# Optimization experiments

Hardware: AMD Instinct MI355X
Metric: run time of the kernel (lower is better)

## Reference

```python
import jax, jax.numpy as jnp
import numpy as np

Nmax = 200
B = 512
LATENT = 128
ENC_H = 256
DEC_H = 512
M = 20


def setup_inputs() -> dict:
    key = jax.random.key(0)
    ks = jax.random.split(key, 16)

    def rn(k, shape):
        return jax.random.normal(k, shape, jnp.float32) / np.sqrt(shape[0]).astype(np.float32)

    inp = {}
    inp["x"] = jax.random.normal(ks[0], (Nmax + 1, B, 5), jnp.float32)
    inp["N_s"] = jax.random.randint(ks[1], (B, 1), 0, Nmax, jnp.int32)
    inp["eps"] = jax.random.normal(ks[2], (B, LATENT), jnp.float32)
    # bidirectional encoder LSTM (torch gate order i,f,g,o)
    inp["enc_Wih_f"] = rn(ks[3], (5, 4 * ENC_H))
    inp["enc_Whh_f"] = rn(ks[4], (ENC_H, 4 * ENC_H))
    inp["enc_b_f"] = jnp.zeros((4 * ENC_H,), jnp.float32)
    inp["enc_Wih_b"] = rn(ks[5], (5, 4 * ENC_H))
    inp["enc_Whh_b"] = rn(ks[6], (ENC_H, 4 * ENC_H))
    inp["enc_b_b"] = jnp.zeros((4 * ENC_H,), jnp.float32)
    inp["W_mu"] = rn(ks[7], (2 * ENC_H, LATENT))
    inp["b_mu"] = jnp.zeros((LATENT,), jnp.float32)
    inp["W_logvar"] = rn(ks[8], (2 * ENC_H, LATENT))
    inp["b_logvar"] = jnp.zeros((LATENT,), jnp.float32)
    # decoder
    inp["W_fc_in"] = rn(ks[9], (LATENT, 2 * DEC_H))
    inp["b_fc_in"] = jnp.zeros((2 * DEC_H,), jnp.float32)
    inp["dec_Wih"] = rn(ks[10], (5 + LATENT, 4 * DEC_H))
    inp["dec_Whh"] = rn(ks[11], (DEC_H, 4 * DEC_H))
    inp["dec_b"] = jnp.zeros((4 * DEC_H,), jnp.float32)
    inp["W_out"] = rn(ks[12], (DEC_H, 6 * M + 3))
    inp["b_out"] = jnp.zeros((6 * M + 3,), jnp.float32)
    return inp


def _lstm_step(h, c, x, Wih, Whh, b):
    g = x @ Wih + h @ Whh + b
    i, f, gg, o = jnp.split(g, 4, axis=-1)
    c = jax.nn.sigmoid(f) * c + jax.nn.sigmoid(i) * jnp.tanh(gg)
    h = jax.nn.sigmoid(o) * jnp.tanh(c)
    return h, c


def reference(x, N_s, eps, enc_Wih_f, enc_Whh_f, enc_b_f, enc_Wih_b, enc_Whh_b, enc_b_b,
              W_mu, b_mu, W_logvar, b_logvar, W_fc_in, b_fc_in,
              dec_Wih, dec_Whh, dec_b, W_out, b_out):
    Bn = x.shape[1]
    dt = x.dtype

    # ---- bidirectional LSTM encoder -> mean, logvar ----
    def run(xs, Wih, Whh, b):
        H = Whh.shape[0]
        def step(hc, xt):
            h, c = _lstm_step(hc[0], hc[1], xt, Wih, Whh, b)
            return (h, c), None
        (h, _), _ = jax.lax.scan(step, (jnp.zeros((Bn, H), dt), jnp.zeros((Bn, H), dt)), xs)
        return h

    h_enc = jnp.concatenate([run(x, enc_Wih_f, enc_Whh_f, enc_b_f),
                             run(x[::-1], enc_Wih_b, enc_Whh_b, enc_b_b)], axis=-1)
    mean = h_enc @ W_mu + b_mu
    logvar = h_enc @ W_logvar + b_logvar
    z = mean + jnp.exp(logvar / 2) * eps  # reparameterize

    # decoder initial state from z
    hc0 = jnp.tanh(z @ W_fc_in + b_fc_in)
    h0, c0 = jnp.split(hc0, 2, axis=-1)

    # ---- make_target ----
    lens = N_s[:, 0]  # [B]
    mask = (jnp.arange(Nmax + 1)[:, None] < lens[None, :]).astype(dt)  # [Nmax+1, B]
    dx, dy = x[..., 0], x[..., 1]

    stroke0 = jnp.broadcast_to(jnp.array([0, 0, 1, 0, 0], dt), (Bn, 5))  # SOS
    empty = jnp.array([0, 0, 0, 0, 1], dt)
    steps = jnp.arange(1, Nmax)
    xs = (x[1:Nmax], dx[1:Nmax], dy[1:Nmax], mask[1:Nmax], steps)

    def step(carry, inp):
        h, c, prev, pl, ol = carry
        xt, dxt, dyt, mt, i = inp
        h, c = _lstm_step(h, c, jnp.concatenate([prev, z], axis=-1), dec_Wih, dec_Whh, dec_b)
        y = h @ W_out + b_out  # [B, 6M+3]
        mix = y[:, :6 * M].reshape(Bn, M, 6)
        pi_h, mu_x, mu_y, sx_h, sy_h, rho_h = (mix[..., j] for j in range(6))
        q_h = y[:, 6 * M:]
        pi = jax.nn.softmax(pi_h, axis=-1)
        sx, sy, rho = jnp.exp(sx_h), jnp.exp(sy_h), jnp.tanh(rho_h)
        # pen reconstruction loss (categorical CE over p1,p2,p3)
        pl = pl + (-(xt[:, 2:] * jax.nn.log_softmax(q_h, axis=-1)).sum() / Bn) / Nmax
        # offset reconstruction loss (bivariate GMM NLL, masked)
        zx = (dxt[:, None] - mu_x) / sx
        zy = (dyt[:, None] - mu_y) / sy
        om = 1.0 - rho * rho
        pdf = jnp.exp(-(zx * zx + zy * zy - 2.0 * rho * zx * zy) / (2.0 * om)) / (2.0 * jnp.pi * sx * sy * jnp.sqrt(om))
        gmm = (pi * pdf).sum(axis=-1)
        ol = ol + (-(mt * jnp.log(gmm + 1e-6)).sum() / Bn) / Nmax
        # deterministic next stroke: expected offsets + argmax pen state
        q = jax.nn.softmax(q_h, axis=-1)
        stroke = jnp.concatenate([(pi * mu_x).sum(-1, keepdims=True),
                                  (pi * mu_y).sum(-1, keepdims=True),
                                  jax.nn.one_hot(jnp.argmax(q, axis=-1), 3, dtype=dt)], axis=-1)
        stroke = jnp.where((i > lens)[:, None], empty, stroke)  # per-index stroke masking
        return (h, c, stroke, pl, ol), stroke

    init = (h0, c0, stroke0, jnp.zeros((), dt), jnp.zeros((), dt))
    (_, _, _, pen_loss, offset_loss), strokes = jax.lax.scan(step, init, xs)
    # torch returns strokes[1:]; row Nmax is never written -> zeros
    strokes = jnp.concatenate([strokes, jnp.zeros((1, Bn, 5), dt)], axis=0)  # [Nmax, B, 5]
    return strokes, offset_loss, pen_loss, mean, logvar
```

## Files before the change

kernel.cpp:

```cpp
#include <hip/hip_runtime.h>
#include <hip/hip_bf16.h>
#include <math.h>

#define NMIX 20

typedef unsigned short u16;
typedef unsigned int   u32;
typedef unsigned long long u64;
typedef __bf16 bfx8 __attribute__((ext_vector_type(8)));
typedef float  fx4  __attribute__((ext_vector_type(4)));

#define MFMA16(a,b,c) __builtin_amdgcn_mfma_f32_16x16x32_bf16((a),(b),(c),0,0,0)

__device__ __forceinline__ float sigm(float x){ return 1.0f/(1.0f+__expf(-x)); }
__device__ __forceinline__ u16 f2bf(float x){ u32 u=__float_as_uint(x); return (u16)((u + 0x7fffu + ((u>>16)&1u))>>16); }
__device__ __forceinline__ float bf2f(u16 h){ return __uint_as_float(((u32)h)<<16); }
__device__ __forceinline__ u32 packh(float v){ u16 hh=f2bf(v); return ((u32)hh<<16) | (u32)f2bf(v - bf2f(hh)); }

__device__ __forceinline__ u64 ald64(const u64* p){ return __hip_atomic_load(p,__ATOMIC_RELAXED,__HIP_MEMORY_SCOPE_AGENT); }
__device__ __forceinline__ u32 ald32(const u32* p){ return __hip_atomic_load(p,__ATOMIC_RELAXED,__HIP_MEMORY_SCOPE_AGENT); }
__device__ __forceinline__ void ast64(u64* p,u64 v){ __hip_atomic_store(p,v,__ATOMIC_RELAXED,__HIP_MEMORY_SCOPE_AGENT); }
__device__ __forceinline__ void ast32(u32* p,u32 v){ __hip_atomic_store(p,v,__ATOMIC_RELAXED,__HIP_MEMORY_SCOPE_AGENT); }

__device__ __forceinline__ void poll(const int* f,int mask,int tok){
  const int idx=(threadIdx.x&63)&mask;
  for(;;){ int v=__hip_atomic_load(f+idx,__ATOMIC_RELAXED,__HIP_MEMORY_SCOPE_AGENT);
    if(__all(v>=tok)) break; __builtin_amdgcn_s_sleep(1); }
  __atomic_signal_fence(__ATOMIC_SEQ_CST);
}

__global__ __launch_bounds__(256) void prep_split_T(const float* __restrict__ src,
                                                    u16* dhi, u16* dlo, int K, int Nsrc, int Nout) {
    int idx = blockIdx.x * 256 + threadIdx.x;
    if (idx >= Nout * K) return;
    int n = idx / K, k = idx - n * K;
    float v = (n < Nsrc) ? src[k * Nsrc + n] : 0.0f;
    u16 hh = f2bf(v);
    dhi[idx] = hh;
    dlo[idx] = f2bf(v - bf2f(hh));
}

__global__ __launch_bounds__(256,1) void enc_persist(
    const float* __restrict__ x,
    const float* __restrict__ Wih_f, const float* __restrict__ b_f,
    const float* __restrict__ Wih_b, const float* __restrict__ b_b,
    const u16* __restrict__ encT, u32* __restrict__ he32, int* __restrict__ encF)
{
    __shared__ u16 AH[32*256];
    __shared__ u16 AL[32*256];
    __shared__ float xL[160];

    const int bx=blockIdx.x, dir=bx>>6, jx=(bx>>4)&3, rt=bx&15;
    const int j0=jx*64, row0=rt*32;
    int* ef = encF + (dir*16+rt)*32;
    const u16* wTh = encT + dir*524288;
    const u16* wTl = wTh + 262144;
    const float* Wih = dir? Wih_b : Wih_f;
    const float* bias= dir? b_b : b_f;

    const int tid=threadIdx.x, wv=tid>>6, lane=tid&63;
    const int ln15=lane&15, kq=lane>>4;
    const int jc = wv*16+ln15;
    const int arow = tid>>3, agran = tid&7;

    float wih[5][4], bi4[4];
#pragma unroll
    for(int g=0; g<4; ++g){
        bi4[g] = bias[g*256 + j0 + jc];
#pragma unroll
        for(int i=0;i<5;++i) wih[i][g] = Wih[i*1024 + g*256 + j0 + jc];
    }
    float c16[2][4] = {};

#pragma unroll 1
    for (int t=0; t<=200; ++t) {
      const int pb=t&1;
      const u32* hp = he32 + (pb*2+dir)*131072;
      u32* hn = he32 + ((pb^1)*2+dir)*131072;
      const int ts = dir ? 200-t : t;
      for (int i = tid; i < 160; i += 256) xL[i] = x[ts*2560 + row0*5 + i];
      poll(ef, 3, t);

      u64 q[16];
      {
        const u64* s = (const u64*)(hp + (size_t)(row0+arow)*256);
#pragma unroll
        for(int i=0;i<16;++i) q[i] = ald64(s + i*8 + agran);
      }
#pragma unroll
      for(int i=0;i<16;++i){
        u32 pe=(u32)q[i], po=(u32)(q[i]>>32);
        int ui = i*8 + agran;
        int off = arow*256 + (((ui>>2) ^ (arow&7))<<3) + (ui&3)*2;
        *(u32*)&AH[off] = (pe>>16) | (po & 0xffff0000u);
        *(u32*)&AL[off] = (pe & 0xffffu) | (po<<16);
      }
      __syncthreads();

      fx4 acc[2][4] = {};
#pragma unroll
      for(int ch=0; ch<8; ++ch){
        bfx8 ah[2], al[2];
#pragma unroll
        for(int rta=0;rta<2;++rta){
          int off = (rta*16+ln15)*256 + (((ch*4+kq)^(ln15&7))<<3);
          ah[rta]=*(const bfx8*)&AH[off]; al[rta]=*(const bfx8*)&AL[off];
        }
#pragma unroll
        for(int nt=0;nt<4;++nt){
          size_t bo=(size_t)(nt*256 + j0 + jc)*256 + ch*32 + kq*8;
          bfx8 bh=*(const bfx8*)&wTh[bo], bl=*(const bfx8*)&wTl[bo];
#pragma unroll
          for(int rta=0;rta<2;++rta){
            acc[rta][nt]=MFMA16(ah[rta],bh,acc[rta][nt]);
            acc[rta][nt]=MFMA16(ah[rta],bl,acc[rta][nt]);
            acc[rta][nt]=MFMA16(al[rta],bh,acc[rta][nt]);}}
      }
#pragma unroll
      for(int rta=0;rta<2;++rta)
#pragma unroll
      for(int r2=0;r2<4;++r2){
        const int rl=rta*16+kq*4+r2;
        float gv[4];
#pragma unroll
        for(int g=0;g<4;++g){
          float s2=acc[rta][g][r2]+bi4[g];
#pragma unroll
          for(int i=0;i<5;++i) s2+=xL[rl*5+i]*wih[i][g];
          gv[g]=s2;}
        float cv=c16[rta][r2];
        cv=sigm(gv[1])*cv+sigm(gv[0])*tanhf(gv[2]);
        c16[rta][r2]=cv;
        float hv2=sigm(gv[3])*tanhf(cv);
        ast32(&hn[(row0+rl)*256 + j0 + jc], packh(hv2));
      }
      __syncthreads();
      if(tid==0) __hip_atomic_store(&ef[jx], t+1, __ATOMIC_RELAXED, __HIP_MEMORY_SCOPE_AGENT);
    }
}

__global__ __launch_bounds__(256) void latent1(
    const u32* __restrict__ he32,
    const float* __restrict__ W_mu, const float* __restrict__ b_mu,
    const float* __restrict__ W_lv, const float* __restrict__ b_lv,
    const float* __restrict__ eps, float* z, float* out)
{
    __shared__ float hs[16 * 512];
    const int row0 = blockIdx.x * 16;
    const int tid = threadIdx.x;
    const u32* hf = he32 + 2*131072;
    const u32* hb = he32 + 3*131072;
    for (int i = tid; i < 8192; i += 256) {
        int r = i >> 9, col = i & 511;
        int gi = (row0 + r) * 256;
        u32 p = (col < 256) ? hf[gi + col] : hb[gi + (col - 256)];
        hs[i] = bf2f((u16)(p >> 16)) + bf2f((u16)p);
    }
    __syncthreads();
    for (int p = tid; p < 2048; p += 256) {
        int r = p >> 7, cc = p & 127;
        const float* hr = hs + r * 512;
        float m = 0, lv = 0;
#pragma unroll 8
        for (int k = 0; k < 512; ++k) {
            float hv = hr[k];
            m  += hv * W_mu[k * 128 + cc];
            lv += hv * W_lv[k * 128 + cc];
        }
        m += b_mu[cc]; lv += b_lv[cc];
        int b = row0 + r;
        out[512002 + b * 128 + cc] = m;
        out[577538 + b * 128 + cc] = lv;
        z[b * 128 + cc] = m + __expf(0.5f * lv) * eps[b * 128 + cc];
    }
}

__global__ __launch_bounds__(256) void latent2(
    const float* __restrict__ z, const float* __restrict__ W_fc, const float* __restrict__ b_fc,
    const float* __restrict__ dWih, const float* __restrict__ dec_b,
    u32* __restrict__ hd32, float* c_d, float* zpre)
{
    __shared__ float zs[16 * 128];
    const int row0 = blockIdx.y * 16;
    const int tid = threadIdx.x;
    {
        float4* dst = (float4*)zs;
        const float4* src = (const float4*)(z + row0 * 128);
        for (int i = tid; i < 512; i += 256) dst[i] = src[i];
    }
    __syncthreads();
    const int colbase = blockIdx.x * 128;
    for (int p = tid; p < 16 * 128; p += 256) {
        int r = p >> 7, cl = p & 127;
        int col = colbase + cl;
        const float* zr = zs + r * 128;
        int b = row0 + r;
        if (col < 1024) {
            float acc = 0;
#pragma unroll 8
            for (int k = 0; k < 128; ++k) acc += zr[k] * W_fc[k * 1024 + col];
            float v = tanhf(acc + b_fc[col]);
            if (col < 512) hd32[b * 512 + col] = packh(v);
            else           c_d[b * 512 + (col - 512)] = v;
        } else {
            int n = col - 1024;
            float acc = 0;
#pragma unroll 8
            for (int k = 0; k < 128; ++k) acc += zr[k] * dWih[(5 + k) * 2048 + n];
            zpre[b * 2048 + n] = acc + dec_b[n];
        }
    }
}

__global__ __launch_bounds__(256,1) void dec_persist(
    const float* __restrict__ x, const int* __restrict__ N_s,
    const float* __restrict__ dec_Wih, const float* __restrict__ b_out,
    const u16* __restrict__ decT, const u16* __restrict__ woutT,
    const float* __restrict__ zpre, const float* __restrict__ c_init,
    u32* __restrict__ hd32, float* __restrict__ sxsG, float* __restrict__ out,
    int* __restrict__ decHF, int* __restrict__ decSF)
{
    __shared__ u16 AH[32*256];
    __shared__ u16 AL[32*256];
    __shared__ float sxsL[32*8];
    __shared__ float xtL[160];
    __shared__ float yL[32*132];
    __shared__ int  lenL[32];
    __shared__ float redL[64];

    const int bx=blockIdx.x, jx=bx>>4, rt=bx&15;
    const int row0=rt*32;
    int* hF = decHF + rt*32;
    int* sF = decSF + rt*32;
    const u16* wHh = decT;
    const u16* wHl = decT + 1048576;
    const u16* wOh = woutT;
    const u16* wOl = woutT + 65536;

    const int tid=threadIdx.x, wv=tid>>6, lane=tid&63;
    const int ln15=lane&15, kq=lane>>4;
    const int jc = wv*16+ln15;
    const int arow = tid>>3, agran = tid&7;

    auto LOADA=[&](const u32* hp, int b, u64* q){
        const u64* s = (const u64*)(hp + (size_t)(row0+arow)*512 + b*256);
#pragma unroll
        for(int i=0;i<16;++i) q[i] = ald64(s + i*8 + agran);
    };
    auto WRITEA=[&](const u64* q){
#pragma unroll
        for(int i=0;i<16;++i){
            u32 pe=(u32)q[i], po=(u32)(q[i]>>32);
            int ui = i*8 + agran;
            int off = arow*256 + (((ui>>2) ^ (arow&7))<<3) + (ui&3)*2;
            *(u32*)&AH[off] = (pe>>16) | (po & 0xffff0000u);
            *(u32*)&AL[off] = (pe & 0xffffu) | (po<<16);
        }
    };

    if (jx < 8) {
        const int j0 = jx*64;
        float dw[5][4], zp[2][4][4], c16[2][4];
#pragma unroll
        for(int g=0;g<4;++g)
#pragma unroll
        for(int i=0;i<5;++i) dw[i][g] = dec_Wih[i*2048 + g*512 + j0 + jc];
#pragma unroll
        for(int rta=0;rta<2;++rta)
#pragma unroll
        for(int r2=0;r2<4;++r2){
            const int R = row0 + rta*16 + kq*4 + r2;
            c16[rta][r2] = c_init[(size_t)R*512 + j0 + jc];
#pragma unroll
            for(int g=0;g<4;++g) zp[rta][r2][g] = zpre[(size_t)R*2048 + g*512 + j0 + jc];
        }
        for (int i = tid; i < 256; i += 256) sxsL[i] = ((i&7)==2) ? 1.0f : 0.0f;
        __syncthreads();

#pragma unroll 1
        for (int s = 0; s < 199; ++s) {
            const u32* hp = hd32 + (s&1)*262144;
            u32* hn = hd32 + ((s&1)^1)*262144;
            poll(hF, 7, s);

            fx4 acc[2][4] = {};
            u64 q[16], q2[16];
            LOADA(hp,0,q);
            WRITEA(q); __syncthreads();
            LOADA(hp,1,q2);
#pragma unroll
            for(int b=0;b<2;++b){
                if(b){ __syncthreads(); WRITEA(q2); __syncthreads(); }
#pragma unroll
                for(int ch=0; ch<8; ++ch){
                    bfx8 ah[2], al[2];
#pragma unroll
                    for(int rta=0;rta<2;++rta){
                        int off = (rta*16+ln15)*256 + (((ch*4+kq)^(ln15&7))<<3);
                        ah[rta]=*(const bfx8*)&AH[off]; al[rta]=*(const bfx8*)&AL[off];
                    }
#pragma unroll
                    for(int nt=0;nt<4;++nt){
                        size_t bo=(size_t)(nt*512 + j0 + jc)*512 + b*256 + ch*32 + kq*8;
                        bfx8 bh=*(const bfx8*)&wHh[bo], bl=*(const bfx8*)&wHl[bo];
#pragma unroll
                        for(int rta=0;rta<2;++rta){
                            acc[rta][nt]=MFMA16(ah[rta],bh,acc[rta][nt]);
                            acc[rta][nt]=MFMA16(ah[rta],bl,acc[rta][nt]);
                            acc[rta][nt]=MFMA16(al[rta],bh,acc[rta][nt]);}}
                }
            }
            if (s > 0) {
                poll(sF, 0, s);
                if (tid < 32) {
                    const u64* p = (const u64*)sxsG + (rt*32 + tid)*4;
                    u64 v0 = ald64(p), v1 = ald64(p+1);
                    u32 v2 = ald32((const u32*)(p+2));
                    sxsL[tid*8+0] = __uint_as_float((u32)v0);
                    sxsL[tid*8+1] = __uint_as_float((u32)(v0>>32));
                    sxsL[tid*8+2] = __uint_as_float((u32)v1);
                    sxsL[tid*8+3] = __uint_as_float((u32)(v1>>32));
                    sxsL[tid*8+4] = __uint_as_float(v2);
                }
            }
            __syncthreads();
#pragma unroll
            for(int rta=0;rta<2;++rta)
#pragma unroll
            for(int r2=0;r2<4;++r2){
                const int rl=rta*16+kq*4+r2;
                float gv[4];
#pragma unroll
                for(int g=0;g<4;++g){
                    float s2=acc[rta][g][r2]+zp[rta][r2][g];
#pragma unroll
                    for(int i=0;i<5;++i) s2+=sxsL[rl*8+i]*dw[i][g];
                    gv[g]=s2;}
                float cv=c16[rta][r2];
                cv=sigm(gv[1])*cv+sigm(gv[0])*tanhf(gv[2]);
                c16[rta][r2]=cv;
                float hv2=sigm(gv[3])*tanhf(cv);
                ast32(&hn[(size_t)(row0+rl)*512 + j0 + jc], packh(hv2));
            }
            __syncthreads();
            if(tid==0) __hip_atomic_store(&hF[jx], s+1, __ATOMIC_RELAXED, __HIP_MEMORY_SCOPE_AGENT);
        }
    } else {
        if (tid < 32) lenL[tid] = N_s[row0 + tid];
        float bo2[2];
#pragma unroll
        for(int nt=0;nt<2;++nt){ int col=wv*32+nt*16+ln15; bo2[nt] = (col<123)? b_out[col] : 0.0f; }
        __syncthreads();

#pragma unroll 1
        for (int s = 1; s < 200; ++s) {
            const u32* hp = hd32 + (s&1)*262144;
            for (int i = tid; i < 160; i += 256) xtL[i] = x[s*2560 + row0*5 + i];
            poll(hF, 7, s);

            fx4 acc[2][2] = {};
            u64 q[16], q2[16];
            LOADA(hp,0,q);
            WRITEA(q); __syncthreads();
            LOADA(hp,1,q2);
#pragma unroll
            for(int b=0;b<2;++b){
                if(b){ __syncthreads(); WRITEA(q2); __syncthreads(); }
#pragma unroll
                for(int ch=0; ch<8; ++ch){
                    bfx8 ah[2], al[2];
#pragma unroll
                    for(int rta=0;rta<2;++rta){
                        int off = (rta*16+ln15)*256 + (((ch*4+kq)^(ln15&7))<<3);
                        ah[rta]=*(const bfx8*)&AH[off]; al[rta]=*(const bfx8*)&AL[off];
                    }
#pragma unroll
                    for(int nt=0;nt<2;++nt){
                        size_t bo=(size_t)(wv*32 + nt*16 + ln15)*512 + b*256 + ch*32 + kq*8;
                        bfx8 bh=*(const bfx8*)&wOh[bo], bl=*(const bfx8*)&wOl[bo];
#pragma unroll
                        for(int rta=0;rta<2;++rta){
                            acc[rta][nt]=MFMA16(ah[rta],bh,acc[rta][nt]);
                            acc[rta][nt]=MFMA16(ah[rta],bl,acc[rta][nt]);
                            acc[rta][nt]=MFMA16(al[rta],bh,acc[rta][nt]);}}
                }
            }
#pragma unroll
            for(int rta=0;rta<2;++rta)
#pragma unroll
            for(int nt=0;nt<2;++nt)
#pragma unroll
            for(int r2=0;r2<4;++r2)
                yL[(rta*16+kq*4+r2)*132 + wv*32+nt*16+ln15] = acc[rta][nt][r2] + bo2[nt];
            __syncthreads();
            {
                const int row = tid>>3, sub = tid&7;
                const float* yr = &yL[row*132];
                const float dxv = xtL[row*5], dyv = xtL[row*5+1];
                float pm = -1e30f;
                for (int cg = sub; cg < NMIX; cg += 8) pm = fmaxf(pm, yr[cg*6]);
                pm = fmaxf(pm, __shfl_xor(pm, 1));
                pm = fmaxf(pm, __shfl_xor(pm, 2));
                pm = fmaxf(pm, __shfl_xor(pm, 4));
                float S = 0, gp = 0, gx = 0, gy = 0;
                for (int cg = sub; cg < NMIX; cg += 8) {
                    float ph = yr[cg*6], mux = yr[cg*6+1], muy = yr[cg*6+2];
                    float ssx = __expf(yr[cg*6+3]), ssy = __expf(yr[cg*6+4]);
                    float rho = tanhf(yr[cg*6+5]);
                    float e = __expf(ph - pm);
                    float zx = (dxv - mux)/ssx, zy = (dyv - muy)/ssy;
                    float om = 1.0f - rho*rho;
                    float pdf = __expf(-(zx*zx + zy*zy - 2.0f*rho*zx*zy)/(2.0f*om))
                                * (0.15915494309189535f/(ssx*ssy*sqrtf(om)));
                    S += e; gp += e*pdf; gx += e*mux; gy += e*muy;
                }
#pragma unroll
                for (int off = 1; off < 8; off <<= 1) {
                    S += __shfl_xor(S, off); gp += __shfl_xor(gp, off);
                    gx += __shfl_xor(gx, off); gy += __shfl_xor(gy, off);
                }
                if (sub == 0) {
                    const int b = row0 + row;
                    float q0v = yr[120], q1v = yr[121], q2v = yr[122];
                    int len = lenL[row];
                    int am = 0; float bv = q0v;
                    if (q1v > bv) { bv = q1v; am = 1; }
                    if (q2v > bv) { bv = q2v; am = 2; }
                    float s0,s1,s2,s3,s4;
                    if (s > len) { s0=s1=s2=s3=0.0f; s4=1.0f; }
                    else { s0=gx/S; s1=gy/S; s2=(am==0); s3=(am==1); s4=(am==2); }
                    u64* p = (u64*)sxsG + (rt*32+row)*4;
                    ast64(p,   (u64)__float_as_uint(s0) | ((u64)__float_as_uint(s1)<<32));
                    ast64(p+1, (u64)__float_as_uint(s2) | ((u64)__float_as_uint(s3)<<32));
                    ast32(((u32*)p)+4, __float_as_uint(s4));
                    float qm = fmaxf(q0v, fmaxf(q1v, q2v));
                    float lse = qm + logf(__expf(q0v-qm)+__expf(q1v-qm)+__expf(q2v-qm));
                    float pl = -(xtL[row*5+2]*(q0v-lse) + xtL[row*5+3]*(q1v-lse) + xtL[row*5+4]*(q2v-lse));
                    float ol = (s < len) ? -logf(gp/S + 1e-6f) : 0.0f;
                    float* so = out + (s-1)*2560 + b*5;
                    so[0]=s0; so[1]=s1; so[2]=s2; so[3]=s3; so[4]=s4;
                    redL[row] = pl; redL[32+row] = ol;
                }
            }
            __syncthreads();
            if (tid == 0) {
                float spl=0, sol=0;
                for (int r=0;r<32;++r){ spl+=redL[r]; sol+=redL[32+r]; }
                atomicAdd(out + 512001, spl * (1.0f/102400.0f));
                atomicAdd(out + 512000, sol * (1.0f/102400.0f));
                __hip_atomic_store(&sF[0], s, __ATOMIC_RELAXED, __HIP_MEMORY_SCOPE_AGENT);
            }
        }
    }
}

extern "C" void kernel_launch(void* const* d_in, const int* in_sizes, int n_in,
                              void* d_out_, int out_size, void* d_ws, size_t ws_size,
                              hipStream_t stream) {
    const float* x         = (const float*)d_in[0];
    const int*   N_s       = (const int*)  d_in[1];
    const float* eps       = (const float*)d_in[2];
    const float* enc_Wih_f = (const float*)d_in[3];
    const float* enc_Whh_f = (const float*)d_in[4];
    const float* enc_b_f   = (const float*)d_in[5];
    const float* enc_Wih_b = (const float*)d_in[6];
    const float* enc_Whh_b = (const float*)d_in[7];
    const float* enc_b_b   = (const float*)d_in[8];
    const float* W_mu      = (const float*)d_in[9];
    const float* b_mu      = (const float*)d_in[10];
    const float* W_logvar  = (const float*)d_in[11];
    const float* b_logvar  = (const float*)d_in[12];
    const float* W_fc_in   = (const float*)d_in[13];
    const float* b_fc_in   = (const float*)d_in[14];
    const float* dec_Wih   = (const float*)d_in[15];
    const float* dec_Whh   = (const float*)d_in[16];
    const float* dec_b     = (const float*)d_in[17];
    const float* W_out     = (const float*)d_in[18];
    const float* b_out     = (const float*)d_in[19];
    float* out = (float*)d_out_;
    float* ws  = (float*)d_ws;

    float* c_d   = ws + 0;
    float* zpre  = ws + 262144;
    float* z     = ws + 1310720;
    float* sxsG  = ws + 1376256;
    int*   flags = (int*)(ws + 1380352);
    u32*   hd32  = (u32*)(ws + 1382400);
    u32*   he32  = (u32*)(ws + 1906688);
    u16*   encT  = (u16*)(ws + 2430976);
    u16*   decT  = (u16*)(ws + 2955264);
    u16*   woutT = (u16*)(ws + 4003840);
    int* encF  = flags;
    int* decHF = flags + 1024;
    int* decSF = flags + 1536;

    hipMemsetAsync(he32, 0, 262144 * sizeof(u32), stream);
    hipMemsetAsync(flags, 0, 2048 * sizeof(int), stream);
    hipMemsetAsync(out + 509440, 0, 2562 * sizeof(float), stream);

    prep_split_T<<<1024, 256, 0, stream>>>(enc_Whh_f, encT,          encT + 262144,  256, 1024, 1024);
    prep_split_T<<<1024, 256, 0, stream>>>(enc_Whh_b, encT + 524288, encT + 786432,  256, 1024, 1024);
    prep_split_T<<<4096, 256, 0, stream>>>(dec_Whh,   decT,          decT + 1048576, 512, 2048, 2048);
    prep_split_T<<<256,  256, 0, stream>>>(W_out,     woutT,         woutT + 65536,  512, 123, 128);

    enc_persist<<<128, 256, 0, stream>>>(x, enc_Wih_f, enc_b_f, enc_Wih_b, enc_b_b, encT, he32, encF);
    latent1<<<32, 256, 0, stream>>>(he32, W_mu, b_mu, W_logvar, b_logvar, eps, z, out);
    latent2<<<dim3(24, 32), 256, 0, stream>>>(z, W_fc_in, b_fc_in, dec_Wih, dec_b, hd32, c_d, zpre);
    dec_persist<<<144, 256, 0, stream>>>(x, N_s, dec_Wih, b_out, decT, woutT, zpre, c_d,
                                         hd32, sxsG, out, decHF, decSF);
}
```

Before: 7.144 ms.

## Fuse output-head computation into every decoder cell block, dropping separate output blocks

Before, the decoder used 8 cell blocks per row tile plus one dedicated output-head block per tile. The cell blocks waited on a second flag until the output block had published the next stroke input through global memory. Now each of the 128 blocks computes the output projection and mixture/argmax logic itself, redundantly, and keeps the stroke input in shared memory. This removes one cross-block flag handshake and a global round trip from each step's critical path. The cost is extra MFMA work and GMM math in every block, with only block jx==0 writing outputs and losses.

```diff
diff --git a/kernel.cpp b/kernel.cpp
--- a/kernel.cpp
+++ b/kernel.cpp
@@ -18,8 +18,6 @@
 __device__ __forceinline__ u32 packh(float v){ u16 hh=f2bf(v); return ((u32)hh<<16) | (u32)f2bf(v - bf2f(hh)); }
 
 __device__ __forceinline__ u64 ald64(const u64* p){ return __hip_atomic_load(p,__ATOMIC_RELAXED,__HIP_MEMORY_SCOPE_AGENT); }
-__device__ __forceinline__ u32 ald32(const u32* p){ return __hip_atomic_load(p,__ATOMIC_RELAXED,__HIP_MEMORY_SCOPE_AGENT); }
-__device__ __forceinline__ void ast64(u64* p,u64 v){ __hip_atomic_store(p,v,__ATOMIC_RELAXED,__HIP_MEMORY_SCOPE_AGENT); }
 __device__ __forceinline__ void ast32(u32* p,u32 v){ __hip_atomic_store(p,v,__ATOMIC_RELAXED,__HIP_MEMORY_SCOPE_AGENT); }
 
 __device__ __forceinline__ void poll(const int* f,int mask,int tok){
@@ -217,21 +215,19 @@
     const float* __restrict__ dec_Wih, const float* __restrict__ b_out,
     const u16* __restrict__ decT, const u16* __restrict__ woutT,
     const float* __restrict__ zpre, const float* __restrict__ c_init,
-    u32* __restrict__ hd32, float* __restrict__ sxsG, float* __restrict__ out,
-    int* __restrict__ decHF, int* __restrict__ decSF)
+    u32* __restrict__ hd32, float* __restrict__ out, int* __restrict__ decHF)
 {
     __shared__ u16 AH[32*256];
     __shared__ u16 AL[32*256];
+    __shared__ float yL[32*132];
     __shared__ float sxsL[32*8];
     __shared__ float xtL[160];
-    __shared__ float yL[32*132];
     __shared__ int  lenL[32];
     __shared__ float redL[64];
 
     const int bx=blockIdx.x, jx=bx>>4, rt=bx&15;
-    const int row0=rt*32;
+    const int j0=jx*64, row0=rt*32;
     int* hF = decHF + rt*32;
-    int* sF = decSF + rt*32;
     const u16* wHh = decT;
     const u16* wHl = decT + 1048576;
     const u16* wOh = woutT;
@@ -258,47 +254,54 @@
         }
     };
 
-    if (jx < 8) {
-        const int j0 = jx*64;
-        float dw[5][4], zp[2][4][4], c16[2][4];
-#pragma unroll
-        for(int g=0;g<4;++g)
-#pragma unroll
-        for(int i=0;i<5;++i) dw[i][g] = dec_Wih[i*2048 + g*512 + j0 + jc];
-#pragma unroll
-        for(int rta=0;rta<2;++rta)
-#pragma unroll
-        for(int r2=0;r2<4;++r2){
-            const int R = row0 + rta*16 + kq*4 + r2;
-            c16[rta][r2] = c_init[(size_t)R*512 + j0 + jc];
-#pragma unroll
-            for(int g=0;g<4;++g) zp[rta][r2][g] = zpre[(size_t)R*2048 + g*512 + j0 + jc];
-        }
-        for (int i = tid; i < 256; i += 256) sxsL[i] = ((i&7)==2) ? 1.0f : 0.0f;
-        __syncthreads();
+    float dw[5][4], zp[2][4][4], c16[2][4], bo2[2];
+#pragma unroll
+    for(int g=0;g<4;++g)
+#pragma unroll
+    for(int i=0;i<5;++i) dw[i][g] = dec_Wih[i*2048 + g*512 + j0 + jc];
+#pragma unroll
+    for(int rta=0;rta<2;++rta)
+#pragma unroll
+    for(int r2=0;r2<4;++r2){
+        const int R = row0 + rta*16 + kq*4 + r2;
+        c16[rta][r2] = c_init[(size_t)R*512 + j0 + jc];
+#pragma unroll
+        for(int g=0;g<4;++g) zp[rta][r2][g] = zpre[(size_t)R*2048 + g*512 + j0 + jc];
+    }
+#pragma unroll
+    for(int nt=0;nt<2;++nt){ int col=wv*32+nt*16+ln15; bo2[nt] = (col<123)? b_out[col] : 0.0f; }
+    if (tid < 32) lenL[tid] = N_s[row0 + tid];
+    for (int i = tid; i < 256; i += 256) sxsL[i] = ((i&7)==2) ? 1.0f : 0.0f;
+    __syncthreads();
 
 #pragma unroll 1
-        for (int s = 0; s < 199; ++s) {
-            const u32* hp = hd32 + (s&1)*262144;
-            u32* hn = hd32 + ((s&1)^1)*262144;
-            poll(hF, 7, s);
-
-            fx4 acc[2][4] = {};
-            u64 q[16], q2[16];
-            LOADA(hp,0,q);
-            WRITEA(q); __syncthreads();
-            LOADA(hp,1,q2);
-#pragma unroll
-            for(int b=0;b<2;++b){
-                if(b){ __syncthreads(); WRITEA(q2); __syncthreads(); }
-#pragma unroll
-                for(int ch=0; ch<8; ++ch){
-                    bfx8 ah[2], al[2];
-#pragma unroll
-                    for(int rta=0;rta<2;++rta){
-                        int off = (rta*16+ln15)*256 + (((ch*4+kq)^(ln15&7))<<3);
-                        ah[rta]=*(const bfx8*)&AH[off]; al[rta]=*(const bfx8*)&AL[off];
-                    }
+    for (int s = 0; s <= 199; ++s) {
+        const bool do_cell = (s < 199);
+        const bool do_y = (s > 0);
+        if (s == 199 && jx != 0) return;
+        const u32* hp = hd32 + (s&1)*262144;
+        u32* hn = hd32 + ((s&1)^1)*262144;
+        for (int i = tid; i < 160; i += 256) xtL[i] = x[s*2560 + row0*5 + i];
+        poll(hF, 7, s);
+
+        fx4 acc[2][4] = {};
+        fx4 accy[2][2] = {};
+        u64 q[16], q2[16];
+        LOADA(hp,0,q);
+        WRITEA(q); __syncthreads();
+        LOADA(hp,1,q2);
+#pragma unroll
+        for(int b=0;b<2;++b){
+            if(b){ __syncthreads(); WRITEA(q2); __syncthreads(); }
+#pragma unroll
+            for(int ch=0; ch<8; ++ch){
+                bfx8 ah[2], al[2];
+#pragma unroll
+                for(int rta=0;rta<2;++rta){
+                    int off = (rta*16+ln15)*256 + (((ch*4+kq)^(ln15&7))<<3);
+                    ah[rta]=*(const bfx8*)&AH[off]; al[rta]=*(const bfx8*)&AL[off];
+                }
+                if (do_cell) {
 #pragma unroll
                     for(int nt=0;nt<4;++nt){
                         size_t bo=(size_t)(nt*512 + j0 + jc)*512 + b*256 + ch*32 + kq*8;
@@ -309,89 +312,29 @@
                             acc[rta][nt]=MFMA16(ah[rta],bl,acc[rta][nt]);
                             acc[rta][nt]=MFMA16(al[rta],bh,acc[rta][nt]);}}
                 }
-            }
-            if (s > 0) {
-                poll(sF, 0, s);
-                if (tid < 32) {
-                    const u64* p = (const u64*)sxsG + (rt*32 + tid)*4;
-                    u64 v0 = ald64(p), v1 = ald64(p+1);
-                    u32 v2 = ald32((const u32*)(p+2));
-                    sxsL[tid*8+0] = __uint_as_float((u32)v0);
-                    sxsL[tid*8+1] = __uint_as_float((u32)(v0>>32));
-                    sxsL[tid*8+2] = __uint_as_float((u32)v1);
-                    sxsL[tid*8+3] = __uint_as_float((u32)(v1>>32));
-                    sxsL[tid*8+4] = __uint_as_float(v2);
-                }
-            }
-            __syncthreads();
-#pragma unroll
-            for(int rta=0;rta<2;++rta)
-#pragma unroll
-            for(int r2=0;r2<4;++r2){
-                const int rl=rta*16+kq*4+r2;
-                float gv[4];
-#pragma unroll
-                for(int g=0;g<4;++g){
-                    float s2=acc[rta][g][r2]+zp[rta][r2][g];
-#pragma unroll
-                    for(int i=0;i<5;++i) s2+=sxsL[rl*8+i]*dw[i][g];
-                    gv[g]=s2;}
-                float cv=c16[rta][r2];
-                cv=sigm(gv[1])*cv+sigm(gv[0])*tanhf(gv[2]);
-                c16[rta][r2]=cv;
-                float hv2=sigm(gv[3])*tanhf(cv);
-                ast32(&hn[(size_t)(row0+rl)*512 + j0 + jc], packh(hv2));
-            }
-            __syncthreads();
-            if(tid==0) __hip_atomic_store(&hF[jx], s+1, __ATOMIC_RELAXED, __HIP_MEMORY_SCOPE_AGENT);
-        }
-    } else {
-        if (tid < 32) lenL[tid] = N_s[row0 + tid];
-        float bo2[2];
-#pragma unroll
-        for(int nt=0;nt<2;++nt){ int col=wv*32+nt*16+ln15; bo2[nt] = (col<123)? b_out[col] : 0.0f; }
-        __syncthreads();
-
-#pragma unroll 1
-        for (int s = 1; s < 200; ++s) {
-            const u32* hp = hd32 + (s&1)*262144;
-            for (int i = tid; i < 160; i += 256) xtL[i] = x[s*2560 + row0*5 + i];
-            poll(hF, 7, s);
-
-            fx4 acc[2][2] = {};
-            u64 q[16], q2[16];
-            LOADA(hp,0,q);
-            WRITEA(q); __syncthreads();
-            LOADA(hp,1,q2);
-#pragma unroll
-            for(int b=0;b<2;++b){
-                if(b){ __syncthreads(); WRITEA(q2); __syncthreads(); }
-#pragma unroll
-                for(int ch=0; ch<8; ++ch){
-                    bfx8 ah[2], al[2];
-#pragma unroll
-                    for(int rta=0;rta<2;++rta){
-                        int off = (rta*16+ln15)*256 + (((ch*4+kq)^(ln15&7))<<3);
-                        ah[rta]=*(const bfx8*)&AH[off]; al[rta]=*(const bfx8*)&AL[off];
-                    }
+                if (do_y) {
 #pragma unroll
                     for(int nt=0;nt<2;++nt){
                         size_t bo=(size_t)(wv*32 + nt*16 + ln15)*512 + b*256 + ch*32 + kq*8;
                         bfx8 bh=*(const bfx8*)&wOh[bo], bl=*(const bfx8*)&wOl[bo];
 #pragma unroll
                         for(int rta=0;rta<2;++rta){
-                            acc[rta][nt]=MFMA16(ah[rta],bh,acc[rta][nt]);
-                            acc[rta][nt]=MFMA16(ah[rta],bl,acc[rta][nt]);
-                            acc[rta][nt]=MFMA16(al[rta],bh,acc[rta][nt]);}}
+                            accy[rta][nt]=MFMA16(ah[rta],bh,accy[rta][nt]);
+                            accy[rta][nt]=MFMA16(ah[rta],bl,accy[rta][nt]);
+                            accy[rta][nt]=MFMA16(al[rta],bh,accy[rta][nt]);}}
                 }
             }
+        }
+        __syncthreads();
+
+        if (do_y) {
 #pragma unroll
             for(int rta=0;rta<2;++rta)
 #pragma unroll
             for(int nt=0;nt<2;++nt)
 #pragma unroll
             for(int r2=0;r2<4;++r2)
-                yL[(rta*16+kq*4+r2)*132 + wv*32+nt*16+ln15] = acc[rta][nt][r2] + bo2[nt];
+                yL[(rta*16+kq*4+r2)*132 + wv*32+nt*16+ln15] = accy[rta][nt][r2] + bo2[nt];
             __syncthreads();
             {
                 const int row = tid>>3, sub = tid&7;
@@ -429,27 +372,49 @@
                     float s0,s1,s2,s3,s4;
                     if (s > len) { s0=s1=s2=s3=0.0f; s4=1.0f; }
                     else { s0=gx/S; s1=gy/S; s2=(am==0); s3=(am==1); s4=(am==2); }
-                    u64* p = (u64*)sxsG + (rt*32+row)*4;
-                    ast64(p,   (u64)__float_as_uint(s0) | ((u64)__float_as_uint(s1)<<32));
-                    ast64(p+1, (u64)__float_as_uint(s2) | ((u64)__float_as_uint(s3)<<32));
-                    ast32(((u32*)p)+4, __float_as_uint(s4));
-                    float qm = fmaxf(q0v, fmaxf(q1v, q2v));
-                    float lse = qm + logf(__expf(q0v-qm)+__expf(q1v-qm)+__expf(q2v-qm));
-                    float pl = -(xtL[row*5+2]*(q0v-lse) + xtL[row*5+3]*(q1v-lse) + xtL[row*5+4]*(q2v-lse));
-                    float ol = (s < len) ? -logf(gp/S + 1e-6f) : 0.0f;
-                    float* so = out + (s-1)*2560 + b*5;
-                    so[0]=s0; so[1]=s1; so[2]=s2; so[3]=s3; so[4]=s4;
-                    redL[row] = pl; redL[32+row] = ol;
+                    sxsL[row*8+0]=s0; sxsL[row*8+1]=s1; sxsL[row*8+2]=s2;
+                    sxsL[row*8+3]=s3; sxsL[row*8+4]=s4;
+                    if (jx == 0) {
+                        float qm = fmaxf(q0v, fmaxf(q1v, q2v));
+                        float lse = qm + logf(__expf(q0v-qm)+__expf(q1v-qm)+__expf(q2v-qm));
+                        float pl = -(xtL[row*5+2]*(q0v-lse) + xtL[row*5+3]*(q1v-lse) + xtL[row*5+4]*(q2v-lse));
+                        float ol = (s < len) ? -logf(gp/S + 1e-6f) : 0.0f;
+                        float* so = out + (s-1)*2560 + b*5;
+                        so[0]=s0; so[1]=s1; so[2]=s2; so[3]=s3; so[4]=s4;
+                        redL[row] = pl; redL[32+row] = ol;
+                    }
                 }
             }
             __syncthreads();
-            if (tid == 0) {
+            if (jx == 0 && tid == 0) {
                 float spl=0, sol=0;
                 for (int r=0;r<32;++r){ spl+=redL[r]; sol+=redL[32+r]; }
                 atomicAdd(out + 512001, spl * (1.0f/102400.0f));
                 atomicAdd(out + 512000, sol * (1.0f/102400.0f));
-                __hip_atomic_store(&sF[0], s, __ATOMIC_RELAXED, __HIP_MEMORY_SCOPE_AGENT);
             }
+        }
+
+        if (do_cell) {
+#pragma unroll
+            for(int rta=0;rta<2;++rta)
+#pragma unroll
+            for(int r2=0;r2<4;++r2){
+                const int rl=rta*16+kq*4+r2;
+                float gv[4];
+#pragma unroll
+                for(int g=0;g<4;++g){
+                    float s2=acc[rta][g][r2]+zp[rta][r2][g];
+#pragma unroll
+                    for(int i=0;i<5;++i) s2+=sxsL[rl*8+i]*dw[i][g];
+                    gv[g]=s2;}
+                float cv=c16[rta][r2];
+                cv=sigm(gv[1])*cv+sigm(gv[0])*tanhf(gv[2]);
+                c16[rta][r2]=cv;
+                float hv2=sigm(gv[3])*tanhf(cv);
+                ast32(&hn[(size_t)(row0+rl)*512 + j0 + jc], packh(hv2));
+            }
+            __syncthreads();
+            if(tid==0) __hip_atomic_store(&hF[jx], s+1, __ATOMIC_RELAXED, __HIP_MEMORY_SCOPE_AGENT);
         }
     }
 }
@@ -483,7 +448,6 @@
     float* c_d   = ws + 0;
     float* zpre  = ws + 262144;
     float* z     = ws + 1310720;
-    float* sxsG  = ws + 1376256;
     int*   flags = (int*)(ws + 1380352);
     u32*   hd32  = (u32*)(ws + 1382400);
     u32*   he32  = (u32*)(ws + 1906688);
@@ -492,7 +456,6 @@
     u16*   woutT = (u16*)(ws + 4003840);
     int* encF  = flags;
     int* decHF = flags + 1024;
-    int* decSF = flags + 1536;
 
     hipMemsetAsync(he32, 0, 262144 * sizeof(u32), stream);
     hipMemsetAsync(flags, 0, 2048 * sizeof(int), stream);
@@ -506,6 +469,6 @@
     enc_persist<<<128, 256, 0, stream>>>(x, enc_Wih_f, enc_b_f, enc_Wih_b, enc_b_b, encT, he32, encF);
     latent1<<<32, 256, 0, stream>>>(he32, W_mu, b_mu, W_logvar, b_logvar, eps, z, out);
     latent2<<<dim3(24, 32), 256, 0, stream>>>(z, W_fc_in, b_fc_in, dec_Wih, dec_b, hd32, c_d, zpre);
-    dec_persist<<<144, 256, 0, stream>>>(x, N_s, dec_Wih, b_out, decT, woutT, zpre, c_d,
-                                         hd32, sxsG, out, decHF, decSF);
-}
+    dec_persist<<<128, 256, 0, stream>>>(x, N_s, dec_Wih, b_out, decT, woutT, zpre, c_d,
+                                         hd32, out, decHF);
+}
```

Result: slower. 9.029 ms (+26.4%).
